# Kernel tuning notes

Hardware: AMD Instinct MI355X
Metric: run time of the kernel (lower is better)

The kernel has to match this reference:

```python
import jax, jax.numpy as jnp
import numpy as np

N_NODES = 50000
N_EDGES = 800000
N_PRED = 100000  # pos and neg each
D_IN = 256
D_HID = 128  # hard-coded hidden width of conv1
D_OUT = 128  # out_channels


def _lin_params(key, fan_in, fan_out, dtype=jnp.float32):
    kw, kb = jax.random.split(key)
    s = 1.0 / np.sqrt(fan_in)
    W = jax.random.uniform(kw, (fan_in, fan_out), dtype, -s, s)
    b = jax.random.uniform(kb, (fan_out,), dtype, -s, s)
    return W, b


def setup_inputs() -> dict:
    key = jax.random.key(0)
    ks = jax.random.split(key, 16)
    inp = {
        "x": jax.random.normal(ks[0], (N_NODES, D_IN), jnp.float32),
        "edge_index": jax.random.randint(ks[1], (2, N_EDGES), 0, N_NODES, jnp.int64),
        "pos_edge_index": jax.random.randint(ks[2], (2, N_PRED), 0, N_NODES, jnp.int64),
        "neg_edge_index": jax.random.randint(ks[3], (2, N_PRED), 0, N_NODES, jnp.int64),
    }
    # conv1: TransformerConv(D_IN -> D_HID), heads=1, root_weight=True
    inp["Wq1"], inp["bq1"] = _lin_params(ks[4], D_IN, D_HID)
    inp["Wk1"], inp["bk1"] = _lin_params(ks[5], D_IN, D_HID)
    inp["Wv1"], inp["bv1"] = _lin_params(ks[6], D_IN, D_HID)
    inp["Ws1"], inp["bs1"] = _lin_params(ks[7], D_IN, D_HID)
    # conv2: TransformerConv(D_HID -> D_OUT)
    inp["Wq2"], inp["bq2"] = _lin_params(ks[8], D_HID, D_OUT)
    inp["Wk2"], inp["bk2"] = _lin_params(ks[9], D_HID, D_OUT)
    inp["Wv2"], inp["bv2"] = _lin_params(ks[10], D_HID, D_OUT)
    inp["Ws2"], inp["bs2"] = _lin_params(ks[11], D_HID, D_OUT)
    # final edge scorer Linear(D_OUT, 1)
    inp["Wl"], inp["bl"] = _lin_params(ks[12], D_OUT, 1)
    return inp


def _transformer_conv(x, Wq, bq, Wk, bk, Wv, bv, Ws, bs, src, dst, n_nodes):
    # PyG TransformerConv, heads=1, concat=True, root_weight=True, no edge attrs.
    C = Wq.shape[1]
    q = x @ Wq + bq  # [N, C] queries (destination side)
    k = x @ Wk + bk  # [N, C] keys (source side)
    v = x @ Wv + bv  # [N, C] values (source side)
    # per-edge attention logits, softmax normalized over incoming edges of dst
    alpha = jnp.einsum("ec,ec->e", q[dst], k[src]) / jnp.sqrt(jnp.asarray(C, x.dtype))
    amax = jax.lax.stop_gradient(jax.ops.segment_max(alpha, dst, num_segments=n_nodes))
    ex = jnp.exp(alpha - amax[dst])
    den = jax.ops.segment_sum(ex, dst, num_segments=n_nodes)
    w = ex / den[dst]  # [E]
    agg = jax.ops.segment_sum(v[src] * w[:, None], dst, num_segments=n_nodes)  # [N, C]
    return agg + (x @ Ws + bs)  # skip connection (lin_skip)


def reference(x, edge_index, pos_edge_index, neg_edge_index,
              Wq1, bq1, Wk1, bk1, Wv1, bv1, Ws1, bs1,
              Wq2, bq2, Wk2, bk2, Wv2, bv2, Ws2, bs2,
              Wl, bl):
    src, dst = edge_index[0], edge_index[1]
    h = _transformer_conv(x, Wq1, bq1, Wk1, bk1, Wv1, bv1, Ws1, bs1, src, dst, N_NODES)
    h = jax.nn.relu(h)
    h = _transformer_conv(h, Wq2, bq2, Wk2, bk2, Wv2, bv2, Ws2, bs2, src, dst, N_NODES)
    ei = jnp.concatenate([pos_edge_index, neg_edge_index], axis=-1)  # [2, 2*N_PRED]
    prod = h[ei[0]] * h[ei[1]]  # [2*N_PRED, D_OUT]
    return (prod @ Wl + bl).squeeze(-1)  # [2*N_PRED]
```

## Files before the change

kernel.cpp:

```cpp
#include <hip/hip_runtime.h>
#include <cstdint>
#include <cstddef>

#define NN 50000
#define NE 800000
#define NP 100000
#define NB 196

#define CVT_BLOCKS   12500
#define PACKW_BLOCKS 1024
#define HIST_BLOCKS  3125

typedef _Float16 h8v __attribute__((ext_vector_type(8)));
typedef _Float16 h4v __attribute__((ext_vector_type(4)));
typedef _Float16 h2v __attribute__((ext_vector_type(2)));
typedef float    f4v __attribute__((ext_vector_type(4)));

#define ATTN_SCALE 0.088388347648318447f

__device__ inline void load_lds16(const void* gptr, void* ldsptr) {
  __builtin_amdgcn_global_load_lds(
      (const __attribute__((address_space(1))) void*)gptr,
      (__attribute__((address_space(3))) void*)ldsptr, 16, 0, 0);
}

__device__ inline float dot8(h8v a, h8v b, float c) {
  union U { h8v v; h2v p[4]; };
  U ua; ua.v = a;
  U ub; ub.v = b;
#if __has_builtin(__builtin_amdgcn_fdot2)
  c = __builtin_amdgcn_fdot2(ua.p[0], ub.p[0], c, false);
  c = __builtin_amdgcn_fdot2(ua.p[1], ub.p[1], c, false);
  c = __builtin_amdgcn_fdot2(ua.p[2], ub.p[2], c, false);
  c = __builtin_amdgcn_fdot2(ua.p[3], ub.p[3], c, false);
#else
#pragma unroll
  for (int j = 0; j < 8; ++j) c = fmaf((float)a[j], (float)b[j], c);
#endif
  return c;
}

__global__ __launch_bounds__(256) void prep_kernel(
    const float* __restrict__ x, _Float16* __restrict__ Xf,
    const float* __restrict__ Wq1, const float* __restrict__ Wk1,
    const float* __restrict__ Wv1, const float* __restrict__ Ws1,
    const float* __restrict__ Wq2, const float* __restrict__ Wk2,
    const float* __restrict__ Wv2, const float* __restrict__ Ws2,
    _Float16* __restrict__ WT1, _Float16* __restrict__ WT2,
    const int* __restrict__ dst, int* __restrict__ deg, int* __restrict__ rank) {
  int b = blockIdx.x;
  int tid = threadIdx.x;
  if (b < CVT_BLOCKS) {
    int i = b * 256 + tid;
    float4 xv = ((const float4*)x)[i];
    h4v o = {(_Float16)xv.x, (_Float16)xv.y, (_Float16)xv.z, (_Float16)xv.w};
    ((h4v*)Xf)[i] = o;
  } else if (b < CVT_BLOCKS + PACKW_BLOCKS) {
    int bb = b - CVT_BLOCKS;
    if (bb < 512) {
      int n = bb;
      const float* W;
      switch (n >> 7) {
        case 0:  W = Wq1; break;
        case 1:  W = Wk1; break;
        case 2:  W = Wv1; break;
        default: W = Ws1; break;
      }
      WT1[(size_t)n * 256 + tid] = (_Float16)W[(size_t)tid * 128 + (n & 127)];
    } else if (tid < 128) {
      int n = bb - 512;
      const float* W;
      switch (n >> 7) {
        case 0:  W = Wq2; break;
        case 1:  W = Wk2; break;
        case 2:  W = Wv2; break;
        default: W = Ws2; break;
      }
      WT2[(size_t)n * 128 + tid] = (_Float16)W[(size_t)tid * 128 + (n & 127)];
    }
  } else {
    int e = (b - CVT_BLOCKS - PACKW_BLOCKS) * 256 + tid;
    if (e < NE) rank[e] = atomicAdd(&deg[dst[e]], 1);
  }
}

__global__ __launch_bounds__(256) void scan1_kernel(const int* __restrict__ deg,
                                                    int* __restrict__ loc,
                                                    int* __restrict__ bsum, int n) {
  __shared__ int sh[256];
  int tid = threadIdx.x;
  int i = blockIdx.x * 256 + tid;
  int val = (i < n) ? deg[i] : 0;
  sh[tid] = val;
  __syncthreads();
  for (int off = 1; off < 256; off <<= 1) {
    int add = (tid >= off) ? sh[tid - off] : 0;
    __syncthreads();
    sh[tid] += add;
    __syncthreads();
  }
  if (i < n) loc[i] = sh[tid] - val;
  if (tid == 255) bsum[blockIdx.x] = sh[255];
}

__global__ __launch_bounds__(256) void scan23_kernel(const int* __restrict__ loc,
                                                     const int* __restrict__ bsum,
                                                     int* __restrict__ offs,
                                                     int n, int E) {
  __shared__ int sh[256];
  int bid = blockIdx.x, tid = threadIdx.x;
  int pre = 0;
  for (int j = tid; j < bid; j += 256) pre += bsum[j];
  sh[tid] = pre;
  __syncthreads();
  for (int off = 128; off > 0; off >>= 1) {
    if (tid < off) sh[tid] += sh[tid + off];
    __syncthreads();
  }
  int base = sh[0];
  int i = bid * 256 + tid;
  if (i < n) offs[i] = loc[i] + base;
  if (bid == 0 && tid == 0) offs[n] = E;
}

__global__ __launch_bounds__(256) void scatter_kernel(const int* __restrict__ src,
                                                      const int* __restrict__ dst,
                                                      const int* __restrict__ offs,
                                                      const int* __restrict__ rank,
                                                      unsigned short* __restrict__ csr_src,
                                                      int E) {
  int e = blockIdx.x * 256 + threadIdx.x;
  if (e < E) {
    int d = dst[e];
    csr_src[offs[d] + rank[e]] = (unsigned short)src[e];
  }
}

__global__ __launch_bounds__(512) void gemm_all_kernel(
    const _Float16* __restrict__ A, int M, int K,
    const _Float16* __restrict__ BT,
    const float* __restrict__ bq, const float* __restrict__ bk,
    const float* __restrict__ bv, const float* __restrict__ bs,
    _Float16* __restrict__ Oq, _Float16* __restrict__ Okv,
    _Float16* __restrict__ Os) {
  __shared__ _Float16 As[128 * 64];
  __shared__ _Float16 Bs[512 * 64];

  const int tx = threadIdx.x;
  const int w = tx >> 6;
  const int lane = tx & 63;
  const int lr = lane & 15;
  const int q = lane >> 4;
  const int wm = w >> 2;
  const int wn = w & 3;
  const int row0 = blockIdx.x * 128;

  f4v acc[4][8];
#pragma unroll
  for (int i = 0; i < 4; ++i)
#pragma unroll
    for (int j = 0; j < 8; ++j) acc[i][j] = (f4v){0.f, 0.f, 0.f, 0.f};

  for (int k0 = 0; k0 < K; k0 += 64) {
    __syncthreads();
#pragma unroll
    for (int o = 0; o < 2; ++o) {
      int i = o * 8 + w;
      int r = i * 8 + (lane >> 3);
      int cl = (lane & 7) ^ (r & 7);
      int gr = row0 + r;
      if (gr > M - 1) gr = M - 1;
      load_lds16(A + (size_t)gr * K + k0 + cl * 8, &As[i * 8 * 64]);
    }
#pragma unroll
    for (int o = 0; o < 8; ++o) {
      int i = o * 8 + w;
      int r = i * 8 + (lane >> 3);
      int cl = (lane & 7) ^ (r & 7);
      load_lds16(BT + (size_t)r * K + k0 + cl * 8, &Bs[i * 8 * 64]);
    }
    __syncthreads();

#pragma unroll
    for (int kk = 0; kk < 2; ++kk) {
      h8v af[4], bf[8];
#pragma unroll
      for (int t = 0; t < 4; ++t) {
        int row = wm * 64 + t * 16 + lr;
        af[t] = *(const h8v*)&As[row * 64 + (((kk * 4 + q) ^ (row & 7)) * 8)];
      }
#pragma unroll
      for (int u = 0; u < 8; ++u) {
        int col = wn * 128 + u * 16 + lr;
        bf[u] = *(const h8v*)&Bs[col * 64 + (((kk * 4 + q) ^ (col & 7)) * 8)];
      }
#pragma unroll
      for (int mt = 0; mt < 4; ++mt)
#pragma unroll
        for (int nt = 0; nt < 8; ++nt)
          acc[mt][nt] = __builtin_amdgcn_mfma_f32_16x16x32_f16(af[mt], bf[nt],
                                                               acc[mt][nt], 0, 0, 0);
    }
  }

  const float* bp = (wn == 0) ? bq : (wn == 1) ? bk : (wn == 2) ? bv : bs;
#pragma unroll
  for (int half = 0; half < 2; ++half) {
    __syncthreads();
    if (wm == half) {
#pragma unroll
      for (int nt = 0; nt < 8; ++nt) {
        int col = wn * 128 + nt * 16 + lr;
        float bval = bp[nt * 16 + lr];
#pragma unroll
        for (int mt = 0; mt < 4; ++mt)
#pragma unroll
          for (int reg = 0; reg < 4; ++reg) {
            int r = mt * 16 + q * 4 + reg;
            Bs[r * 512 + col] = (_Float16)(acc[mt][nt][reg] + bval);
          }
      }
    }
    __syncthreads();
#pragma unroll
    for (int i = 0; i < 8; ++i) {
      int sl = i * 512 + tx;
      int rr = sl >> 6;
      int c8 = sl & 63;
      int col = c8 * 8;
      int grow = row0 + half * 64 + rr;
      if (grow < M) {
        int p = c8 >> 4;
        int cp = col & 127;
        _Float16* dstp;
        switch (p) {
          case 0:  dstp = Oq  + (size_t)grow * 128 + cp;       break;
          case 1:  dstp = Okv + (size_t)grow * 256 + cp;       break;
          case 2:  dstp = Okv + (size_t)grow * 256 + 128 + cp; break;
          default: dstp = Os  + (size_t)grow * 128 + cp;       break;
        }
        *(h8v*)dstp = *(const h8v*)&Bs[rr * 512 + col];
      }
    }
  }
}

__global__ __launch_bounds__(256) void attn_fused_kernel(
    const _Float16* __restrict__ qf, const _Float16* __restrict__ kvf,
    const _Float16* __restrict__ sf,
    const int* __restrict__ offs, const unsigned short* __restrict__ csr_src,
    _Float16* __restrict__ hf, int n_nodes, int do_relu) {
  int node = (int)((blockIdx.x * 256u + threadIdx.x) >> 6);
  if (node >= n_nodes) return;
  int lane = threadIdx.x & 63;
  int g = lane >> 4;
  int t = lane & 15;

  h8v qv = *(const h8v*)(qf + (size_t)node * 128 + t * 8);
  int beg = offs[node], end = offs[node + 1];

  float den = 0.f;
  float acc[8];
#pragma unroll
  for (int j = 0; j < 8; ++j) acc[j] = 0.f;

  int e = beg + g;
  for (; e + 4 < end; e += 8) {
    int sn0 = csr_src[e];
    int sn1 = csr_src[e + 4];
    const _Float16* r0 = kvf + (size_t)sn0 * 256 + t * 8;
    const _Float16* r1 = kvf + (size_t)sn1 * 256 + t * 8;
    h8v k0 = *(const h8v*)r0, v0 = *(const h8v*)(r0 + 128);
    h8v k1 = *(const h8v*)r1, v1 = *(const h8v*)(r1 + 128);
    float p0 = dot8(qv, k0, 0.f);
    float p1 = dot8(qv, k1, 0.f);
    p0 += __shfl_xor(p0, 1); p1 += __shfl_xor(p1, 1);
    p0 += __shfl_xor(p0, 2); p1 += __shfl_xor(p1, 2);
    p0 += __shfl_xor(p0, 4); p1 += __shfl_xor(p1, 4);
    p0 += __shfl_xor(p0, 8); p1 += __shfl_xor(p1, 8);
    float w0 = __expf(p0 * ATTN_SCALE);
    float w1 = __expf(p1 * ATTN_SCALE);
    den += w0 + w1;
#pragma unroll
    for (int j = 0; j < 8; ++j) {
      acc[j] = fmaf(w0, (float)v0[j], acc[j]);
      acc[j] = fmaf(w1, (float)v1[j], acc[j]);
    }
  }
  if (e < end) {
    int sn0 = csr_src[e];
    const _Float16* r0 = kvf + (size_t)sn0 * 256 + t * 8;
    h8v k0 = *(const h8v*)r0, v0 = *(const h8v*)(r0 + 128);
    float p0 = dot8(qv, k0, 0.f);
    p0 += __shfl_xor(p0, 1);
    p0 += __shfl_xor(p0, 2);
    p0 += __shfl_xor(p0, 4);
    p0 += __shfl_xor(p0, 8);
    float w0 = __expf(p0 * ATTN_SCALE);
    den += w0;
#pragma unroll
    for (int j = 0; j < 8; ++j) acc[j] = fmaf(w0, (float)v0[j], acc[j]);
  }

#pragma unroll
  for (int j = 0; j < 8; ++j) {
    acc[j] += __shfl_xor(acc[j], 16);
    acc[j] += __shfl_xor(acc[j], 32);
  }
  den += __shfl_xor(den, 16);
  den += __shfl_xor(den, 32);

  if (g == 0) {
    float inv = (end > beg) ? 1.f / den : 0.f;
    h8v sk = *(const h8v*)(sf + (size_t)node * 128 + t * 8);
    h8v of;
#pragma unroll
    for (int j = 0; j < 8; ++j) {
      float o = fmaf(acc[j], inv, (float)sk[j]);
      if (do_relu) o = fmaxf(o, 0.f);
      of[j] = (_Float16)o;
    }
    *(h8v*)(hf + (size_t)node * 128 + t * 8) = of;
  }
}

__global__ __launch_bounds__(256) void scorer_kernel(
    const _Float16* __restrict__ hf,
    const int* __restrict__ pos0, const int* __restrict__ pos1,
    const int* __restrict__ neg0, const int* __restrict__ neg1,
    const float* __restrict__ Wl, const float* __restrict__ bl,
    float* __restrict__ out, int npred) {
  int eid = (int)((blockIdx.x * 256u + threadIdx.x) >> 4);
  if (eid >= 2 * npred) return;
  int t = threadIdx.x & 15;

  int a, b;
  if (eid < npred) { a = pos0[eid]; b = pos1[eid]; }
  else             { a = neg0[eid - npred]; b = neg1[eid - npred]; }

  h8v ha = *(const h8v*)(hf + (size_t)a * 128 + t * 8);
  h8v hb = *(const h8v*)(hf + (size_t)b * 128 + t * 8);
  const float4* wp = (const float4*)(Wl + t * 8);
  float4 w0 = wp[0], w1 = wp[1];
  float wl[8] = {w0.x, w0.y, w0.z, w0.w, w1.x, w1.y, w1.z, w1.w};
  float p = 0.f;
#pragma unroll
  for (int j = 0; j < 8; ++j)
    p = fmaf((float)ha[j] * (float)hb[j], wl[j], p);
  p += __shfl_xor(p, 1);
  p += __shfl_xor(p, 2);
  p += __shfl_xor(p, 4);
  p += __shfl_xor(p, 8);
  if (t == 0) out[eid] = p + bl[0];
}

extern "C" void kernel_launch(void* const* d_in, const int* in_sizes, int n_in,
                              void* d_out, int out_size, void* d_ws, size_t ws_size,
                              hipStream_t stream) {
  const float* x   = (const float*)d_in[0];
  const int*   ei  = (const int*)d_in[1];
  const int*   pos = (const int*)d_in[2];
  const int*   neg = (const int*)d_in[3];
  const float* Wq1 = (const float*)d_in[4];  const float* bq1 = (const float*)d_in[5];
  const float* Wk1 = (const float*)d_in[6];  const float* bk1 = (const float*)d_in[7];
  const float* Wv1 = (const float*)d_in[8];  const float* bv1 = (const float*)d_in[9];
  const float* Ws1 = (const float*)d_in[10]; const float* bs1 = (const float*)d_in[11];
  const float* Wq2 = (const float*)d_in[12]; const float* bq2 = (const float*)d_in[13];
  const float* Wk2 = (const float*)d_in[14]; const float* bk2 = (const float*)d_in[15];
  const float* Wv2 = (const float*)d_in[16]; const float* bv2 = (const float*)d_in[17];
  const float* Ws2 = (const float*)d_in[18]; const float* bs2 = (const float*)d_in[19];
  const float* Wl  = (const float*)d_in[20]; const float* bl  = (const float*)d_in[21];
  float* out = (float*)d_out;

  const size_t NODE_C = (size_t)NN * 128;
  char* p = (char*)d_ws;
  _Float16* qf  = (_Float16*)p; p += NODE_C * 2;
  _Float16* kvf = (_Float16*)p; p += NODE_C * 4;
  _Float16* sf  = (_Float16*)p; p += NODE_C * 2;
  _Float16* h1  = (_Float16*)p; p += NODE_C * 2;
  _Float16* h2  = (_Float16*)p; p += NODE_C * 2;
  _Float16* Xf  = (_Float16*)p; p += (size_t)NN * 256 * 2;
  _Float16* WT1 = (_Float16*)p; p += 512 * 256 * 2;
  _Float16* WT2 = (_Float16*)p; p += 512 * 128 * 2;
  int* rank    = (int*)p;      p += (size_t)NE * 4;
  int* deg     = (int*)p;      p += (size_t)NN * 4;
  int* loc     = (int*)p;      p += (size_t)NN * 4;
  int* bsum    = (int*)p;      p += 256 * 4;
  int* offs    = (int*)p;      p += (size_t)(NN + 8) * 4;
  unsigned short* csr_src = (unsigned short*)p; p += (size_t)NE * 2;

  const int* e_src = ei;
  const int* e_dst = ei + NE;

  hipMemsetAsync(deg, 0, NN * sizeof(int), stream);

  prep_kernel<<<CVT_BLOCKS + PACKW_BLOCKS + HIST_BLOCKS, 256, 0, stream>>>(
      x, Xf, Wq1, Wk1, Wv1, Ws1, Wq2, Wk2, Wv2, Ws2, WT1, WT2, e_dst, deg, rank);

  scan1_kernel<<<NB, 256, 0, stream>>>(deg, loc, bsum, NN);
  scan23_kernel<<<NB, 256, 0, stream>>>(loc, bsum, offs, NN, NE);
  scatter_kernel<<<(NE + 255) / 256, 256, 0, stream>>>(e_src, e_dst, offs, rank,
                                                       csr_src, NE);

  int ggrid = (NN + 127) / 128;
  int attn_blocks = (NN * 64 + 255) / 256;

  gemm_all_kernel<<<ggrid, 512, 0, stream>>>(Xf, NN, 256, WT1,
                                             bq1, bk1, bv1, bs1, qf, kvf, sf);
  attn_fused_kernel<<<attn_blocks, 256, 0, stream>>>(
      qf, kvf, sf, offs, csr_src, h1, NN, 1);

  gemm_all_kernel<<<ggrid, 512, 0, stream>>>(h1, NN, 128, WT2,
                                             bq2, bk2, bv2, bs2, qf, kvf, sf);
  attn_fused_kernel<<<attn_blocks, 256, 0, stream>>>(
      qf, kvf, sf, offs, csr_src, h2, NN, 0);

  scorer_kernel<<<(2 * NP * 16 + 255) / 256, 256, 0, stream>>>(
      h2, pos, pos + NP, neg, neg + NP, Wl, bl, out, NP);
}
```

Baseline: 367.5 us.

## Build CSR via two-pass LDS radix sort instead of global atomics

Replaces the global-atomic degree histogram plus scatter with a two-level bucket sort on destination node. The first pass counts per high-byte bucket per block in shared memory, and the second places packed entries into buckets. A third kernel ranks entries within each bucket in shared memory and writes the offsets and source indices. This removes the heavily contended global atomics and the memset, at the cost of an extra temporary array and more kernel launches.

```diff
diff --git a/kernel.cpp b/kernel.cpp
--- a/kernel.cpp
+++ b/kernel.cpp
@@ -5,11 +5,13 @@
 #define NN 50000
 #define NE 800000
 #define NP 100000
-#define NB 196
+
+#define EPB    3125
+#define NBUK   196
 
 #define CVT_BLOCKS   12500
 #define PACKW_BLOCKS 1024
-#define HIST_BLOCKS  3125
+#define RADIX1_BLOCKS 256
 
 typedef _Float16 h8v __attribute__((ext_vector_type(8)));
 typedef _Float16 h4v __attribute__((ext_vector_type(4)));
@@ -47,7 +49,9 @@
     const float* __restrict__ Wq2, const float* __restrict__ Wk2,
     const float* __restrict__ Wv2, const float* __restrict__ Ws2,
     _Float16* __restrict__ WT1, _Float16* __restrict__ WT2,
-    const int* __restrict__ dst, int* __restrict__ deg, int* __restrict__ rank) {
+    const int* __restrict__ dst, unsigned short* __restrict__ erank,
+    int* __restrict__ blockcount) {
+  __shared__ int cnt[256];
   int b = blockIdx.x;
   int tid = threadIdx.x;
   if (b < CVT_BLOCKS) {
@@ -79,8 +83,16 @@
       WT2[(size_t)n * 128 + tid] = (_Float16)W[(size_t)tid * 128 + (n & 127)];
     }
   } else {
-    int e = (b - CVT_BLOCKS - PACKW_BLOCKS) * 256 + tid;
-    if (e < NE) rank[e] = atomicAdd(&deg[dst[e]], 1);
+    int blk = b - CVT_BLOCKS - PACKW_BLOCKS;
+    cnt[tid] = 0;
+    __syncthreads();
+    int base = blk * EPB;
+    for (int i = tid; i < EPB; i += 256) {
+      int e = base + i;
+      erank[e] = (unsigned short)atomicAdd(&cnt[dst[e] >> 8], 1);
+    }
+    __syncthreads();
+    blockcount[tid * 256 + blk] = cnt[tid];
   }
 }
 
@@ -105,7 +117,7 @@
 
 __global__ __launch_bounds__(256) void scan23_kernel(const int* __restrict__ loc,
                                                      const int* __restrict__ bsum,
-                                                     int* __restrict__ offs,
+                                                     int* __restrict__ outv,
                                                      int n, int E) {
   __shared__ int sh[256];
   int bid = blockIdx.x, tid = threadIdx.x;
@@ -119,20 +131,59 @@
   }
   int base = sh[0];
   int i = bid * 256 + tid;
-  if (i < n) offs[i] = loc[i] + base;
-  if (bid == 0 && tid == 0) offs[n] = E;
-}
-
-__global__ __launch_bounds__(256) void scatter_kernel(const int* __restrict__ src,
-                                                      const int* __restrict__ dst,
-                                                      const int* __restrict__ offs,
-                                                      const int* __restrict__ rank,
-                                                      unsigned short* __restrict__ csr_src,
-                                                      int E) {
-  int e = blockIdx.x * 256 + threadIdx.x;
-  if (e < E) {
+  if (i < n) outv[i] = loc[i] + base;
+  if (bid == 0 && tid == 0) outv[n] = E;
+}
+
+__global__ __launch_bounds__(256) void radix2_kernel(
+    const int* __restrict__ src, const int* __restrict__ dst,
+    const int* __restrict__ bcscan, const unsigned short* __restrict__ erank,
+    unsigned* __restrict__ tmp) {
+  int blk = blockIdx.x, tid = threadIdx.x;
+  int base = blk * EPB;
+  for (int i = tid; i < EPB; i += 256) {
+    int e = base + i;
     int d = dst[e];
-    csr_src[offs[d] + rank[e]] = (unsigned short)src[e];
+    int pos = bcscan[(d >> 8) * 256 + blk] + (int)erank[e];
+    tmp[pos] = (unsigned)src[e] | ((unsigned)(d & 255) << 16);
+  }
+}
+
+__global__ __launch_bounds__(256) void radix3_kernel(
+    const unsigned* __restrict__ tmp, const int* __restrict__ bcscan,
+    unsigned short* __restrict__ rank2,
+    int* __restrict__ offs, unsigned short* __restrict__ csr_src) {
+  __shared__ int cnt[256];
+  __shared__ int sh[256];
+  int tid = threadIdx.x, bu = blockIdx.x;
+  cnt[tid] = 0;
+  __syncthreads();
+  int bstart = bcscan[bu * 256];
+  int bend   = bcscan[(bu + 1) * 256];
+  for (int i = bstart + tid; i < bend; i += 256) {
+    unsigned u = tmp[i];
+    rank2[i] = (unsigned short)atomicAdd(&cnt[u >> 16], 1);
+  }
+  __syncthreads();
+  int v = cnt[tid];
+  sh[tid] = v;
+  __syncthreads();
+  for (int off = 1; off < 256; off <<= 1) {
+    int add = (tid >= off) ? sh[tid - off] : 0;
+    __syncthreads();
+    sh[tid] += add;
+    __syncthreads();
+  }
+  int excl = sh[tid] - v;
+  int node = bu * 256 + tid;
+  if (node < NN) offs[node] = bstart + excl;
+  if (bu == 0 && tid == 0) offs[NN] = NE;
+  __syncthreads();
+  cnt[tid] = excl;
+  __syncthreads();
+  for (int i = bstart + tid; i < bend; i += 256) {
+    unsigned u = tmp[i];
+    csr_src[bstart + cnt[u >> 16] + (int)rank2[i]] = (unsigned short)(u & 0xffffu);
   }
 }
 
@@ -382,25 +433,28 @@
   _Float16* Xf  = (_Float16*)p; p += (size_t)NN * 256 * 2;
   _Float16* WT1 = (_Float16*)p; p += 512 * 256 * 2;
   _Float16* WT2 = (_Float16*)p; p += 512 * 128 * 2;
-  int* rank    = (int*)p;      p += (size_t)NE * 4;
-  int* deg     = (int*)p;      p += (size_t)NN * 4;
-  int* loc     = (int*)p;      p += (size_t)NN * 4;
-  int* bsum    = (int*)p;      p += 256 * 4;
-  int* offs    = (int*)p;      p += (size_t)(NN + 8) * 4;
+  unsigned short* erank = (unsigned short*)p; p += (size_t)NE * 2;
+  unsigned short* rank2 = (unsigned short*)p; p += (size_t)NE * 2;
+  unsigned* tmp = (unsigned*)p;  p += (size_t)NE * 4;
+  int* bc     = (int*)p;         p += 65536 * 4;
+  int* bcloc  = (int*)p;         p += 65536 * 4;
+  int* bcbs   = (int*)p;         p += 256 * 4;
+  int* bcscan = (int*)p;         p += 65544 * 4;
+  int* offs   = (int*)p;         p += (size_t)(NN + 8) * 4;
   unsigned short* csr_src = (unsigned short*)p; p += (size_t)NE * 2;
 
   const int* e_src = ei;
   const int* e_dst = ei + NE;
 
-  hipMemsetAsync(deg, 0, NN * sizeof(int), stream);
-
-  prep_kernel<<<CVT_BLOCKS + PACKW_BLOCKS + HIST_BLOCKS, 256, 0, stream>>>(
-      x, Xf, Wq1, Wk1, Wv1, Ws1, Wq2, Wk2, Wv2, Ws2, WT1, WT2, e_dst, deg, rank);
-
-  scan1_kernel<<<NB, 256, 0, stream>>>(deg, loc, bsum, NN);
-  scan23_kernel<<<NB, 256, 0, stream>>>(loc, bsum, offs, NN, NE);
-  scatter_kernel<<<(NE + 255) / 256, 256, 0, stream>>>(e_src, e_dst, offs, rank,
-                                                       csr_src, NE);
+  prep_kernel<<<CVT_BLOCKS + PACKW_BLOCKS + RADIX1_BLOCKS, 256, 0, stream>>>(
+      x, Xf, Wq1, Wk1, Wv1, Ws1, Wq2, Wk2, Wv2, Ws2, WT1, WT2,
+      e_dst, erank, bc);
+
+  scan1_kernel<<<256, 256, 0, stream>>>(bc, bcloc, bcbs, 65536);
+  scan23_kernel<<<256, 256, 0, stream>>>(bcloc, bcbs, bcscan, 65536, NE);
+
+  radix2_kernel<<<256, 256, 0, stream>>>(e_src, e_dst, bcscan, erank, tmp);
+  radix3_kernel<<<NBUK, 256, 0, stream>>>(tmp, bcscan, rank2, offs, csr_src);
 
   int ggrid = (NN + 127) / 128;
   int attn_blocks = (NN * 64 + 255) / 256;
```

New measurement: 350.8 us. 4.5% less time.
